# Performance work log

Hardware: AMD Instinct MI355X
Metric: run time of the kernel (lower is better)

The kernel has to match this reference:

```python
import jax, jax.numpy as jnp
import numpy as np

DIM = 256
HEADS = 8
KS = 3          # deform conv kernel size
N = KS * KS     # sampling points per output pixel
PAD = 1


def conv2d(x, w, b=None, stride=1, padding=0):
    out = jax.lax.conv_general_dilated(
        x, w, (stride, stride), [(padding, padding)] * 2,
        dimension_numbers=('NCHW', 'OIHW', 'NCHW'))
    if b is not None:
        out = out + b[None, :, None, None]
    return out


def deform_conv(x, w_pconv, b_pconv, w_dconv):
    b, c, h, w = x.shape
    offset = conv2d(x, w_pconv, b_pconv, padding=1)      # (b, 2N, h, w)
    off = offset.transpose(0, 2, 3, 1)                   # (b, h, w, 2N); [:N]=x-off, [N:]=y-off
    xp = jnp.pad(x, ((0, 0), (0, 0), (PAD, PAD), (PAD, PAD)))
    hp, wp = h + 2 * PAD, w + 2 * PAD
    r = jnp.arange(-(KS - 1) // 2, (KS - 1) // 2 + 1, dtype=x.dtype)
    pnx, pny = jnp.meshgrid(r, r, indexing='ij')
    # sampling positions, 1-indexed into the padded input (matches the torch ref)
    px = off[..., :N] + pnx.reshape(-1) + jnp.arange(1, h + 1, dtype=x.dtype)[None, :, None, None]
    py = off[..., N:] + pny.reshape(-1) + jnp.arange(1, w + 1, dtype=x.dtype)[None, None, :, None]
    fx = jnp.floor(px)
    fy = jnp.floor(py)
    qlt_x = jnp.clip(fx, 0, hp - 1)
    qlt_y = jnp.clip(fy, 0, wp - 1)
    qrb_x = jnp.clip(fx + 1, 0, hp - 1)
    qrb_y = jnp.clip(fy + 1, 0, wp - 1)
    pxc = jnp.clip(px, 0, hp - 1)
    pyc = jnp.clip(py, 0, wp - 1)
    # bilinear weights (can be negative at clamped borders, as in the torch ref)
    g_lt = (1 + (qlt_x - pxc)) * (1 + (qlt_y - pyc))
    g_rb = (1 - (qrb_x - pxc)) * (1 - (qrb_y - pyc))
    g_lb = (1 + (qlt_x - pxc)) * (1 - (qrb_y - pyc))
    g_rt = (1 - (qrb_x - pxc)) * (1 + (qlt_y - pyc))
    ilt_x = qlt_x.astype(jnp.int32)
    ilt_y = qlt_y.astype(jnp.int32)
    irb_x = qrb_x.astype(jnp.int32)
    irb_y = qrb_y.astype(jnp.int32)

    def gather(xb, ix, iy):
        return xb[:, ix, iy]                              # (c, h, w, N)

    gat = jax.vmap(gather)
    x_lt = gat(xp, ilt_x, ilt_y)
    x_rb = gat(xp, irb_x, irb_y)
    x_lb = gat(xp, ilt_x, irb_y)
    x_rt = gat(xp, irb_x, ilt_y)
    x_off = (g_lt[:, None] * x_lt + g_rb[:, None] * x_rb
             + g_lb[:, None] * x_lb + g_rt[:, None] * x_rt)   # (b, c, h, w, N)
    # 'b c h w (i j) -> b c (h i) (w j)' then ks-strided conv
    x_off = x_off.reshape(b, c, h, w, KS, KS).transpose(0, 1, 2, 4, 3, 5)
    x_off = x_off.reshape(b, c, h * KS, w * KS)
    return conv2d(x_off, w_dconv, None, stride=KS)


def ssa_forward(x, w_pconv, b_pconv, w_dconv, w_qkv, temperature, w_proj):
    b, c, h, w = x.shape
    hw = h * w
    ch = c // HEADS
    q = deform_conv(x, w_pconv, b_pconv, w_dconv)         # (b, c, h, w)
    qkv = jnp.einsum('bchw,oc->bohw', x, w_qkv)           # 1x1 conv, (b, 3c, h, w)
    k = qkv[:, c:2 * c]
    v = qkv[:, 2 * c:]
    q = q.reshape(b, HEADS, ch, hw)
    k = k.reshape(b, HEADS, ch, hw)
    v = v.reshape(b, HEADS, ch, hw)
    k = k / jnp.maximum(jnp.linalg.norm(k, axis=-1, keepdims=True), 1e-12)
    v = v / jnp.maximum(jnp.linalg.norm(v, axis=-1, keepdims=True), 1e-12)
    attn = jnp.einsum('bhcn,bhdn->bhcd', q, k) * temperature[None]   # (b, h, ch, ch)
    attn = jax.nn.softmax(attn, axis=-1)
    out = jnp.einsum('bhcd,bhdn->bhcn', attn, v).reshape(b, c, h, w)
    return jnp.einsum('bchw,oc->bohw', out, w_proj)       # project_out 1x1


def setup_inputs() -> dict:
    key = jax.random.key(0)
    ks = jax.random.split(key, 6)
    B, H, W = 2, 96, 96
    x = jax.random.normal(ks[0], (B, DIM, H, W), jnp.float32)
    w_pconv = jax.random.normal(ks[1], (2 * N, DIM, KS, KS), jnp.float32) * 0.01
    b_pconv = jax.random.normal(ks[2], (2 * N,), jnp.float32) * 0.01
    w_dconv = jax.random.normal(ks[3], (DIM, DIM, KS, KS), jnp.float32) * 0.02
    w_qkv = jax.random.normal(ks[4], (3 * DIM, DIM), jnp.float32) * 0.05
    temperature = jnp.ones((HEADS, 1, 1), jnp.float32)
    w_proj = jax.random.normal(ks[5], (DIM, DIM), jnp.float32) * 0.05
    return dict(x=x, w_pconv=w_pconv, b_pconv=b_pconv, w_dconv=w_dconv,
                w_qkv=w_qkv, temperature=temperature, w_proj=w_proj)


def reference(x, w_pconv, b_pconv, w_dconv, w_qkv, temperature, w_proj):
    return ssa_forward(x, w_pconv, b_pconv, w_dconv, w_qkv, temperature, w_proj)
```

## Files before the change

### kernel.cpp

```cpp
#include <hip/hip_runtime.h>
#include <math.h>

#define BB 2
#define CC 256
#define HW 96
#define PP 9216
#define KO 18
#define HEADS 8
#define NCH 18

typedef short bf16x8 __attribute__((ext_vector_type(8)));
typedef float f32x4 __attribute__((ext_vector_type(4)));

#define NP_O    0UL
#define W2_O    147456UL
#define IDX_O   331776UL
#define WGT_O   995328UL
#define WT2_O   1658880UL
#define WP2_O   2248704UL
#define WQ2_O   2322432UL
#define QP_O    2584576UL
#define KV_O    12021760UL
#define AP_O    21459968UL

__device__ __forceinline__ ushort f2bf_rne(float f) {
    unsigned u = __float_as_uint(f);
    unsigned r = (u + 0x7FFFu + ((u >> 16) & 1u)) >> 16;
    return (ushort)r;
}
__device__ __forceinline__ float bf2f(ushort h) {
    return __uint_as_float(((unsigned)h) << 16);
}

__global__ __launch_bounds__(256) void k_prep_wt(const float* __restrict__ wd,
                                                 ushort* __restrict__ h,
                                                 ushort* __restrict__ lo) {
    int tid = blockIdx.x * 256 + threadIdx.x;
    if (tid >= 9 * 8 * 1024 * 8) return;
    int e = tid & 7;
    int u = (tid >> 3) & 1023;
    int cs = (tid >> 13) & 7;
    int kk = tid >> 16;
    int oh = u >> 6, rem = u & 63;
    int lrow = rem & 15, lhi = rem >> 4;
    int o = oh * 16 + lrow;
    int c = cs * 32 + lhi * 8 + e;
    float v = wd[o * 2304 + c * 9 + kk];
    ushort hh = f2bf_rne(v);
    h[tid] = hh;
    lo[tid] = f2bf_rne(v - bf2f(hh));
}

__global__ __launch_bounds__(256) void k_prep_wp(const float* __restrict__ wp,
                                                 ushort* __restrict__ h,
                                                 ushort* __restrict__ lo) {
    int tid = blockIdx.x * 256 + threadIdx.x;
    if (tid >= 9 * 8 * 128 * 8) return;
    int e = tid & 7;
    int u = (tid >> 3) & 127;
    int cs = (tid >> 10) & 7;
    int kk = tid >> 13;
    int mf = u >> 6, rem = u & 63;
    int lrow = rem & 15, lhi = rem >> 4;
    int o = mf * 16 + lrow;
    int c = cs * 32 + lhi * 8 + e;
    float v = (o < KO) ? wp[(o * 256 + c) * 9 + kk] : 0.f;
    ushort hh = f2bf_rne(v);
    h[tid] = hh;
    lo[tid] = f2bf_rne(v - bf2f(hh));
}

__global__ __launch_bounds__(256) void k_prep_w(const float* __restrict__ W,
                                                ushort* __restrict__ h,
                                                ushort* __restrict__ lo,
                                                int total) {
    int tid = blockIdx.x * 256 + threadIdx.x;
    if (tid >= total) return;
    int e = tid & 7;
    int u = (tid >> 3) & 1023;
    int csg = (tid >> 13) & 7;
    int mt = tid >> 16;
    int rem = u & 63;
    int lrow = rem & 15, lhi = rem >> 4;
    int o = mt * 256 + (u >> 6) * 16 + lrow;
    int c = csg * 32 + lhi * 8 + e;
    float v = W[o * 256 + c];
    ushort hh = f2bf_rne(v);
    h[tid] = hh;
    lo[tid] = f2bf_rne(v - bf2f(hh));
}

__global__ __launch_bounds__(256) void k_xt(const float* __restrict__ x,
                                            float* __restrict__ xT) {
    int pt = blockIdx.x;
    int ct = blockIdx.y;
    int b  = blockIdx.z;
    int t = threadIdx.x;
    __shared__ float T[64][65];
    {
        int c = t >> 2, pq = (t & 3) * 16;
        const float* src = x + ((size_t)b * CC + ct * 64 + c) * PP + pt * 64 + pq;
#pragma unroll
        for (int k2 = 0; k2 < 4; ++k2) {
            float4 v = *(const float4*)&src[k2 * 4];
            T[c][pq + k2 * 4 + 0] = v.x;
            T[c][pq + k2 * 4 + 1] = v.y;
            T[c][pq + k2 * 4 + 2] = v.z;
            T[c][pq + k2 * 4 + 3] = v.w;
        }
    }
    __syncthreads();
    {
        int p = t >> 2, cq = (t & 3) * 16;
        float* dst = xT + ((size_t)b * PP + pt * 64 + p) * CC + ct * 64 + cq;
#pragma unroll
        for (int k2 = 0; k2 < 4; ++k2)
            *(float4*)&dst[k2 * 4] = make_float4(T[cq + k2 * 4 + 0][p], T[cq + k2 * 4 + 1][p],
                                                 T[cq + k2 * 4 + 2][p], T[cq + k2 * 4 + 3][p]);
    }
}

__global__ __launch_bounds__(256) void k_pconv(const float* __restrict__ x,
                                               const ushort* __restrict__ wp2h,
                                               const ushort* __restrict__ wp2l,
                                               float* __restrict__ ppart) {
    int s = blockIdx.x;
    int xcd = s & 7;
    int b = xcd & 1, ks = xcd >> 1;
    int p0 = (s >> 3) * 64;
    int t = threadIdx.x;
    int l = t & 63, w = t >> 6;
    int lrow = l & 15, lhi = l >> 4;
    int p = t & 63, cg = t >> 6;
    __shared__ __align__(16) ushort Sh[64 * 40];
    __shared__ __align__(16) ushort Sl[64 * 40];
    f32x4 acc[2];
    acc[0] = (f32x4)0.f; acc[1] = (f32x4)0.f;
    const float* xb = x + (size_t)b * CC * PP;
    int pix = p0 + p;
    int i_ = pix / 96, j_ = pix % 96;
#pragma unroll 1
    for (int cs = 0; cs < 2; ++cs) {
        int csg = ks * 2 + cs;
        const float* xc0 = xb + (size_t)(csg * 32 + cg * 8) * PP;
#pragma unroll 1
        for (int kk = 0; kk < 9; ++kk) {
            int di = kk / 3 - 1, dj = kk % 3 - 1;
            bool vOK = ((unsigned)(i_ + di) < 96u) && ((unsigned)(j_ + dj) < 96u);
            int poff = pix + di * 96 + dj;
            __syncthreads();
            bf16x8 ah[2], al[2];
#pragma unroll
            for (int mf = 0; mf < 2; ++mf) {
                size_t gi = (((size_t)(kk * 8 + csg)) * 128 + (mf * 64 + l)) * 8;
                ah[mf] = *(const bf16x8*)&wp2h[gi];
                al[mf] = *(const bf16x8*)&wp2l[gi];
            }
            bf16x8 vh, vl;
#pragma unroll
            for (int i = 0; i < 8; ++i) {
                float v = vOK ? xc0[(size_t)i * PP + poff] : 0.f;
                ushort hh = f2bf_rne(v);
                vh[i] = (short)hh;
                vl[i] = (short)f2bf_rne(v - bf2f(hh));
            }
            *(bf16x8*)&Sh[p * 40 + cg * 8] = vh;
            *(bf16x8*)&Sl[p * 40 + cg * 8] = vl;
            __syncthreads();
            bf16x8 Bh = *(const bf16x8*)&Sh[(w * 16 + lrow) * 40 + lhi * 8];
            bf16x8 Bl = *(const bf16x8*)&Sl[(w * 16 + lrow) * 40 + lhi * 8];
#pragma unroll
            for (int mf = 0; mf < 2; ++mf) {
                acc[mf] = __builtin_amdgcn_mfma_f32_16x16x32_bf16(ah[mf], Bh, acc[mf], 0, 0, 0);
                acc[mf] = __builtin_amdgcn_mfma_f32_16x16x32_bf16(ah[mf], Bl, acc[mf], 0, 0, 0);
                acc[mf] = __builtin_amdgcn_mfma_f32_16x16x32_bf16(al[mf], Bh, acc[mf], 0, 0, 0);
            }
        }
    }
    float* pr = ppart + ((size_t)(ks * BB + b) * 32) * PP;
#pragma unroll
    for (int mf = 0; mf < 2; ++mf)
#pragma unroll
        for (int j = 0; j < 4; ++j)
            pr[(size_t)(mf * 16 + lhi * 4 + j) * PP + p0 + w * 16 + lrow] = acc[mf][j];
}

__global__ __launch_bounds__(256) void k_bilin2(const float* __restrict__ pp,
                                                const float* __restrict__ bp,
                                                int4* __restrict__ idx4,
                                                float4* __restrict__ wgt4) {
    int idx = blockIdx.x * 256 + threadIdx.x;
    if (idx >= BB * 9 * PP) return;
    int p = idx % PP;
    int bn = idx / PP;
    int n = bn % 9, b = bn / 9;
    int i = p / 96, j = p % 96;
    float ox = bp[n], oy = bp[n + 9];
#pragma unroll
    for (int k = 0; k < 4; ++k) {
        ox += pp[((size_t)(k * BB + b) * 32 + n) * PP + p];
        oy += pp[((size_t)(k * BB + b) * 32 + n + 9) * PP + p];
    }
    float px = ox + (float)(n / 3 - 1) + (float)(i + 1);
    float py = oy + (float)(n % 3 - 1) + (float)(j + 1);
    float fx = floorf(px), fy = floorf(py);
    float qltx = fminf(fmaxf(fx, 0.f), 97.f);
    float qlty = fminf(fmaxf(fy, 0.f), 97.f);
    float qrbx = fminf(fmaxf(fx + 1.f, 0.f), 97.f);
    float qrby = fminf(fmaxf(fy + 1.f, 0.f), 97.f);
    float pxc = fminf(fmaxf(px, 0.f), 97.f);
    float pyc = fminf(fmaxf(py, 0.f), 97.f);
    float glt = (1.f + (qltx - pxc)) * (1.f + (qlty - pyc));
    float grb = (1.f - (qrbx - pxc)) * (1.f - (qrby - pyc));
    float glb = (1.f + (qltx - pxc)) * (1.f - (qrby - pyc));
    float grt = (1.f - (qrbx - pxc)) * (1.f + (qlty - pyc));
    int x0 = (int)qltx - 1, y0 = (int)qlty - 1;
    int x1 = (int)qrbx - 1, y1 = (int)qrby - 1;
    bool vlt = (x0 >= 0 && x0 < 96 && y0 >= 0 && y0 < 96);
    bool vrb = (x1 >= 0 && x1 < 96 && y1 >= 0 && y1 < 96);
    bool vlb = (x0 >= 0 && x0 < 96 && y1 >= 0 && y1 < 96);
    bool vrt = (x1 >= 0 && x1 < 96 && y0 >= 0 && y0 < 96);
    int4 id;
    id.x = vlt ? x0 * 96 + y0 : 0;
    id.y = vrb ? x1 * 96 + y1 : 0;
    id.z = vlb ? x0 * 96 + y1 : 0;
    id.w = vrt ? x1 * 96 + y0 : 0;
    idx4[idx] = id;
    wgt4[idx] = make_float4(vlt ? glt : 0.f, vrb ? grb : 0.f,
                            vlb ? glb : 0.f, vrt ? grt : 0.f);
}

__global__ __launch_bounds__(256) void k_dconv(const float* __restrict__ xT,
                                               const ushort* __restrict__ wt2h,
                                               const ushort* __restrict__ wt2l,
                                               const int4* __restrict__ idx4,
                                               const float4* __restrict__ wgt4,
                                               float* __restrict__ qpart) {
    int s = blockIdx.x;
    int xcd = s & 7, ib = s >> 3;
    int combo = xcd >> 1;
    int b = combo & 1;
    int half = combo >> 1;
    int ptile = (xcd & 1) * 144 + ib;
    int p0 = ptile * 32;
    int t = threadIdx.x;
    int l = t & 63, w = t >> 6;
    int lrow = l & 15, lhi = l >> 4;
    int obase = w * 64;
    int pl = t & 31, cg = t >> 5;

    __shared__ __align__(16) ushort Sh0[32 * 40], Sl0[32 * 40];
    __shared__ __align__(16) ushort Sh1[32 * 40], Sl1[32 * 40];
    __shared__ int4 Tid[9 * 32];
    __shared__ float4 Twg[9 * 32];

    for (int e = t; e < 9 * 32; e += 256) {
        int kk = e >> 5, pq = e & 31;
        size_t tb = ((size_t)b * 9 + kk) * PP + p0 + pq;
        Tid[e] = idx4[tb];
        Twg[e] = wgt4[tb];
    }

    f32x4 acc[4][2];
#pragma unroll
    for (int mf = 0; mf < 4; ++mf)
#pragma unroll
        for (int nf = 0; nf < 2; ++nf) acc[mf][nf] = (f32x4)0.f;

    const float* xTb = xT + (size_t)b * PP * CC;
    int h4 = half * 4;

    float R[16];
    float4 g4r;

    auto LD = [&](int i) {
        int cs = i / 9, kk = i % 9;
        int csg = h4 + cs;
        int4 id = Tid[kk * 32 + pl];
        g4r = Twg[kk * 32 + pl];
        const float* xt0 = xTb + (size_t)(csg * 32 + cg * 4);
        *(float4*)&R[0]  = *(const float4*)&xt0[(size_t)id.x * CC];
        *(float4*)&R[4]  = *(const float4*)&xt0[(size_t)id.y * CC];
        *(float4*)&R[8]  = *(const float4*)&xt0[(size_t)id.z * CC];
        *(float4*)&R[12] = *(const float4*)&xt0[(size_t)id.w * CC];
    };
    auto CONV = [&](ushort* Sh, ushort* Sl) {
        ushort4 vh, vl;
#pragma unroll
        for (int q = 0; q < 4; ++q) {
            float v = g4r.x * R[q];
            v = fmaf(g4r.y, R[4 + q], v);
            v = fmaf(g4r.z, R[8 + q], v);
            v = fmaf(g4r.w, R[12 + q], v);
            ushort hh = f2bf_rne(v);
            ushort ll = f2bf_rne(v - bf2f(hh));
            if (q == 0)      { vh.x = hh; vl.x = ll; }
            else if (q == 1) { vh.y = hh; vl.y = ll; }
            else if (q == 2) { vh.z = hh; vl.z = ll; }
            else             { vh.w = hh; vl.w = ll; }
        }
        *(ushort4*)&Sh[pl * 40 + cg * 4] = vh;
        *(ushort4*)&Sl[pl * 40 + cg * 4] = vl;
    };
    auto COMPUTE = [&](int i, const ushort* Sh, const ushort* Sl) {
        int cs = i / 9, kk = i % 9;
        int csg = h4 + cs;
        bf16x8 ah[4], al[4];
#pragma unroll
        for (int mf = 0; mf < 4; ++mf) {
            size_t gi = (((size_t)(kk * 8 + csg)) * 1024 + ((w * 4 + mf) * 64 + l)) * 8;
            ah[mf] = *(const bf16x8*)&wt2h[gi];
            al[mf] = *(const bf16x8*)&wt2l[gi];
        }
        bf16x8 Bh2[2], Bl2[2];
#pragma unroll
        for (int nf = 0; nf < 2; ++nf) {
            Bh2[nf] = *(const bf16x8*)&Sh[(nf * 16 + lrow) * 40 + lhi * 8];
            Bl2[nf] = *(const bf16x8*)&Sl[(nf * 16 + lrow) * 40 + lhi * 8];
        }
        __builtin_amdgcn_s_setprio(1);
#pragma unroll
        for (int mf = 0; mf < 4; ++mf)
#pragma unroll
            for (int nf = 0; nf < 2; ++nf) {
                acc[mf][nf] = __builtin_amdgcn_mfma_f32_16x16x32_bf16(ah[mf], Bh2[nf], acc[mf][nf], 0, 0, 0);
                acc[mf][nf] = __builtin_amdgcn_mfma_f32_16x16x32_bf16(ah[mf], Bl2[nf], acc[mf][nf], 0, 0, 0);
                acc[mf][nf] = __builtin_amdgcn_mfma_f32_16x16x32_bf16(al[mf], Bh2[nf], acc[mf][nf], 0, 0, 0);
            }
        __builtin_amdgcn_s_setprio(0);
    };

    __syncthreads();
    LD(0); CONV(Sh0, Sl0);
    LD(1);
    __syncthreads();

#pragma unroll 1
    for (int i0 = 0; i0 < 36; i0 += 2) {
        CONV(Sh1, Sl1);
        if (i0 + 2 < 36) LD(i0 + 2);
        COMPUTE(i0, Sh0, Sl0);
        __syncthreads();
        if (i0 + 2 < 36) CONV(Sh0, Sl0);
        if (i0 + 3 < 36) LD(i0 + 3);
        COMPUTE(i0 + 1, Sh1, Sl1);
        __syncthreads();
    }

    float* qh = qpart + (size_t)half * BB * CC * PP + (size_t)b * CC * PP;
#pragma unroll
    for (int mf = 0; mf < 4; ++mf)
#pragma unroll
        for (int nf = 0; nf < 2; ++nf)
#pragma unroll
            for (int j = 0; j < 4; ++j)
                qh[(size_t)(obase + mf * 16 + lhi * 4 + j) * PP + p0 + nf * 16 + lrow] =
                    acc[mf][nf][j];
}

__global__ __launch_bounds__(256) void k_gemm_bf(const float* __restrict__ Bsrc,
                                                 const ushort* __restrict__ A2h,
                                                 const ushort* __restrict__ A2l,
                                                 float* __restrict__ C,
                                                 int mtiles, int bRowStride, int bRowOff,
                                                 int aBatchStride,
                                                 float* __restrict__ npart) {
    int s = blockIdx.x;
    int xcd = s & 7, ib = s >> 3;
    int b, mt, ptile;
    if (mtiles == 2) {
        int combo = xcd >> 1;
        b = combo & 1; mt = combo >> 1;
        ptile = (xcd & 1) * 72 + ib;
    } else {
        b = xcd >> 2; mt = 0;
        ptile = (xcd & 3) * 36 + ib;
    }
    int p0 = ptile * 64;
    int t = threadIdx.x;
    int l = t & 63, w = t >> 6;
    int lrow = l & 15, lhi = l >> 4;
    int obase = w * 64;
    int p = t & 63, cg = t >> 6;
    __shared__ __align__(16) ushort Sh[64 * 40];
    __shared__ __align__(16) ushort Sl[64 * 40];
    f32x4 acc[4][4];
#pragma unroll
    for (int mf = 0; mf < 4; ++mf)
#pragma unroll
        for (int nf = 0; nf < 4; ++nf) acc[mf][nf] = (f32x4)0.f;
    const float* Bb = Bsrc + ((size_t)b * bRowStride + bRowOff) * PP;
    const ushort* Ah = A2h + (size_t)b * aBatchStride;
    const ushort* Al = A2l + (size_t)b * aBatchStride;
#pragma unroll 1
    for (int csg = 0; csg < 8; ++csg) {
        __syncthreads();
        bf16x8 ah[4], al[4];
#pragma unroll
        for (int mf = 0; mf < 4; ++mf) {
            size_t gi = (((size_t)(mt * 8 + csg)) * 1024 + ((w * 4 + mf) * 64 + l)) * 8;
            ah[mf] = *(const bf16x8*)&Ah[gi];
            al[mf] = *(const bf16x8*)&Al[gi];
        }
        const float* xr = Bb + (size_t)(csg * 32 + cg * 8) * PP + p0 + p;
        bf16x8 vh, vl;
#pragma unroll
        for (int i = 0; i < 8; ++i) {
            float v = xr[(size_t)i * PP];
            ushort hh = f2bf_rne(v);
            vh[i] = (short)hh;
            vl[i] = (short)f2bf_rne(v - bf2f(hh));
        }
        *(bf16x8*)&Sh[p * 40 + cg * 8] = vh;
        *(bf16x8*)&Sl[p * 40 + cg * 8] = vl;
        __syncthreads();
        bf16x8 Bh4[4], Bl4[4];
#pragma unroll
        for (int nf = 0; nf < 4; ++nf) {
            Bh4[nf] = *(const bf16x8*)&Sh[(nf * 16 + lrow) * 40 + lhi * 8];
            Bl4[nf] = *(const bf16x8*)&Sl[(nf * 16 + lrow) * 40 + lhi * 8];
        }
#pragma unroll
        for (int mf = 0; mf < 4; ++mf) {
#pragma unroll
            for (int nf = 0; nf < 4; ++nf) {
                acc[mf][nf] = __builtin_amdgcn_mfma_f32_16x16x32_bf16(ah[mf], Bh4[nf], acc[mf][nf], 0, 0, 0);
                acc[mf][nf] = __builtin_amdgcn_mfma_f32_16x16x32_bf16(ah[mf], Bl4[nf], acc[mf][nf], 0, 0, 0);
                acc[mf][nf] = __builtin_amdgcn_mfma_f32_16x16x32_bf16(al[mf], Bh4[nf], acc[mf][nf], 0, 0, 0);
            }
        }
    }
    float* Cb = C + (size_t)b * (mtiles * 256) * PP;
#pragma unroll
    for (int mf = 0; mf < 4; ++mf)
#pragma unroll
        for (int nf = 0; nf < 4; ++nf)
#pragma unroll
            for (int j = 0; j < 4; ++j)
                Cb[(size_t)(mt * 256 + obase + mf * 16 + lhi * 4 + j) * PP + p0 + nf * 16 + lrow] =
                    acc[mf][nf][j];
    if (npart) {
        float sq[4][4];
#pragma unroll
        for (int mf = 0; mf < 4; ++mf)
#pragma unroll
            for (int j = 0; j < 4; ++j) {
                float v0 = acc[mf][0][j], v1 = acc[mf][1][j];
                float v2 = acc[mf][2][j], v3 = acc[mf][3][j];
                sq[mf][j] = v0 * v0 + v1 * v1 + v2 * v2 + v3 * v3;
            }
#pragma unroll
        for (int m = 1; m <= 8; m <<= 1)
#pragma unroll
            for (int mf = 0; mf < 4; ++mf)
#pragma unroll
                for (int j = 0; j < 4; ++j)
                    sq[mf][j] += __shfl_xor(sq[mf][j], m, 64);
        if (lrow == 0) {
            float* np = npart + ((size_t)(b * 2 + mt) * 144 + ptile) * 256;
#pragma unroll
            for (int mf = 0; mf < 4; ++mf)
#pragma unroll
                for (int j = 0; j < 4; ++j)
                    np[obase + mf * 16 + lhi * 4 + j] = sq[mf][j];
        }
    }
}

__global__ __launch_bounds__(256) void k_attn_part(const float* __restrict__ qp,
                                                   const float* __restrict__ kv,
                                                   float* __restrict__ apart) {
    int ch = blockIdx.x, h = blockIdx.y, b = blockIdx.z;
    int t = threadIdx.x;
    int d = t & 31, cg = t >> 5;
    __shared__ float qs[32][37], ks[32][37];
    float acc[4] = {0.f, 0.f, 0.f, 0.f};
    const float* q0 = qp + ((size_t)b * CC + h * 32) * PP;
    const float* q1 = q0 + (size_t)BB * CC * PP;
    const float* kb = kv + ((size_t)b * 512 + h * 32) * PP;
    int r = t >> 3, cq = (t & 7) * 4;
    for (int po = ch * 512; po < ch * 512 + 512; po += 32) {
        float4 va = *(const float4*)&q0[(size_t)r * PP + po + cq];
        float4 vb = *(const float4*)&q1[(size_t)r * PP + po + cq];
        qs[r][cq + 0] = va.x + vb.x; qs[r][cq + 1] = va.y + vb.y;
        qs[r][cq + 2] = va.z + vb.z; qs[r][cq + 3] = va.w + vb.w;
        float4 vk = *(const float4*)&kb[(size_t)r * PP + po + cq];
        ks[r][cq + 0] = vk.x; ks[r][cq + 1] = vk.y;
        ks[r][cq + 2] = vk.z; ks[r][cq + 3] = vk.w;
        __syncthreads();
#pragma unroll
        for (int pq = 0; pq < 32; ++pq) {
            float kvv = ks[d][pq];
#pragma unroll
            for (int i = 0; i < 4; ++i)
                acc[i] = fmaf(qs[cg * 4 + i][pq], kvv, acc[i]);
        }
        __syncthreads();
    }
    float* ap = apart + (((size_t)(b * 8 + h) * NCH + ch) << 10);
#pragma unroll
    for (int i = 0; i < 4; ++i) ap[(cg * 4 + i) * 32 + d] = acc[i];
}

__global__ __launch_bounds__(256) void k_attn_fin_w2(const float* __restrict__ apart,
                                                     const float* __restrict__ npart,
                                                     const float* __restrict__ temp,
                                                     const float* __restrict__ wproj,
                                                     ushort* __restrict__ w2h,
                                                     ushort* __restrict__ w2l) {
    int h = blockIdx.x, b = blockIdx.y;
    int t = threadIdx.x;
    __shared__ float A[32][33];
    __shared__ float invk[32], invv[32];
    if (t < 64) {
        int mt = t >> 5, row = (t & 31) + h * 32;
        const float* base = npart + ((size_t)(b * 2 + mt) * 144) * 256 + row;
        float ssum = 0.f;
        for (int pt = 0; pt < 144; ++pt) ssum += base[pt * 256];
        float iv = 1.f / fmaxf(sqrtf(ssum), 1e-12f);
        if (mt == 0) invk[t & 31] = iv; else invv[t & 31] = iv;
    }
    const float* ap = apart + ((size_t)(b * 8 + h) * NCH << 10);
    float th = temp[h];
    for (int e = t; e < 1024; e += 256) {
        float s = 0.f;
        for (int chn = 0; chn < NCH; ++chn) s += ap[chn * 1024 + e];
        A[e >> 5][e & 31] = s * th;
    }
    __syncthreads();
    if (t < 32) {
        int c = t;
        float m = -INFINITY;
        float row[32];
#pragma unroll
        for (int d = 0; d < 32; ++d) {
            row[d] = A[c][d] * invk[d];
            m = fmaxf(m, row[d]);
        }
        float sum = 0.f;
#pragma unroll
        for (int d = 0; d < 32; ++d) sum += expf(row[d] - m);
        float inv = 1.f / sum;
#pragma unroll
        for (int d = 0; d < 32; ++d)
            A[c][d] = expf(row[d] - m) * inv * invv[d];
    }
    __syncthreads();
    int o = t;
    float wrow[32];
#pragma unroll
    for (int c = 0; c < 32; ++c) wrow[c] = wproj[o * 256 + h * 32 + c];
    int wq = o >> 6, mf = (o >> 4) & 3, lr = o & 15;
    size_t bb = (size_t)b * 65536;
#pragma unroll
    for (int e = 0; e < 32; ++e) {
        float v = 0.f;
#pragma unroll
        for (int c = 0; c < 32; ++c) v = fmaf(wrow[c], A[c][e], v);
        int lhi = e >> 3, ee = e & 7;
        size_t gi = bb + ((size_t)h * 1024 + ((wq * 4 + mf) * 64 + lhi * 16 + lr)) * 8 + ee;
        ushort hh = f2bf_rne(v);
        w2h[gi] = hh;
        w2l[gi] = f2bf_rne(v - bf2f(hh));
    }
}

extern "C" void kernel_launch(void* const* d_in, const int* in_sizes, int n_in,
                              void* d_out, int out_size, void* d_ws, size_t ws_size,
                              hipStream_t stream) {
    const float* x     = (const float*)d_in[0];
    const float* wp    = (const float*)d_in[1];
    const float* bp    = (const float*)d_in[2];
    const float* wd    = (const float*)d_in[3];
    const float* wqkv  = (const float*)d_in[4];
    const float* temp  = (const float*)d_in[5];
    const float* wproj = (const float*)d_in[6];
    float* out = (float*)d_out;
    float* ws  = (float*)d_ws;

    float* npart  = ws + NP_O;
    ushort* w2h   = (ushort*)(ws + W2_O);
    ushort* w2l   = w2h + 2 * 65536;
    int4*  idx4   = (int4*)(ws + IDX_O);
    float4* wgt4  = (float4*)(ws + WGT_O);
    ushort* wt2h  = (ushort*)(ws + WT2_O);
    ushort* wt2l  = wt2h + 9 * 8 * 1024 * 8;
    ushort* wp2h  = (ushort*)(ws + WP2_O);
    ushort* wp2l  = wp2h + 9 * 8 * 128 * 8;
    ushort* wq2h  = (ushort*)(ws + WQ2_O);
    ushort* wq2l  = wq2h + 2 * 8 * 1024 * 8;
    float* qpart  = ws + QP_O;
    float* ppart  = ws + QP_O;
    float* xT     = ws + KV_O;
    float* kv     = ws + KV_O;
    float* apart  = ws + AP_O;

    k_prep_wt<<<2304, 256, 0, stream>>>(wd, wt2h, wt2l);
    k_prep_wp<<<288, 256, 0, stream>>>(wp, wp2h, wp2l);
    k_prep_w<<<512, 256, 0, stream>>>(wqkv + 256 * 256, wq2h, wq2l, 2 * 65536);
    k_pconv<<<1152, 256, 0, stream>>>(x, wp2h, wp2l, ppart);
    k_bilin2<<<(BB * 9 * PP + 255) / 256, 256, 0, stream>>>(ppart, bp, idx4, wgt4);
    k_xt<<<dim3(144, 4, BB), 256, 0, stream>>>(x, xT);
    k_dconv<<<1152, 256, 0, stream>>>(xT, wt2h, wt2l, idx4, wgt4, qpart);
    k_gemm_bf<<<576, 256, 0, stream>>>(x, wq2h, wq2l, kv, 2, 256, 0, 0, npart);
    k_attn_part<<<dim3(NCH, HEADS, BB), 256, 0, stream>>>(qpart, kv, apart);
    k_attn_fin_w2<<<dim3(HEADS, BB), 256, 0, stream>>>(apart, npart, temp, wproj, w2h, w2l);
    k_gemm_bf<<<288, 256, 0, stream>>>(kv, w2h, w2l, out, 1, 512, 256, 65536, nullptr);
}
```

Baseline: 267.3 us.

## Merge prep and bilinear/transpose launches; deepen dconv gather pipeline to two stages

The three weight-prep kernels become one launch that dispatches by block index, and the bilinear-index kernel and the x transpose kernel are merged into another. This removes launch gaps and lets independent work share one grid. In the deformable conv, the LDS ring grows to four buffers and two gather loads are issued per phase, so gathers for steps i+4 and i+5 are in flight while two MFMA steps run, with one barrier per two steps. The cost is more registers and LDS per block, which may lower occupancy.

```diff
diff --git a/kernel.cpp b/kernel.cpp
--- a/kernel.cpp
+++ b/kernel.cpp
@@ -32,91 +32,56 @@
     return __uint_as_float(((unsigned)h) << 16);
 }
 
-__global__ __launch_bounds__(256) void k_prep_wt(const float* __restrict__ wd,
-                                                 ushort* __restrict__ h,
-                                                 ushort* __restrict__ lo) {
-    int tid = blockIdx.x * 256 + threadIdx.x;
-    if (tid >= 9 * 8 * 1024 * 8) return;
-    int e = tid & 7;
-    int u = (tid >> 3) & 1023;
-    int cs = (tid >> 13) & 7;
-    int kk = tid >> 16;
-    int oh = u >> 6, rem = u & 63;
-    int lrow = rem & 15, lhi = rem >> 4;
-    int o = oh * 16 + lrow;
-    int c = cs * 32 + lhi * 8 + e;
-    float v = wd[o * 2304 + c * 9 + kk];
-    ushort hh = f2bf_rne(v);
-    h[tid] = hh;
-    lo[tid] = f2bf_rne(v - bf2f(hh));
-}
-
-__global__ __launch_bounds__(256) void k_prep_wp(const float* __restrict__ wp,
-                                                 ushort* __restrict__ h,
-                                                 ushort* __restrict__ lo) {
-    int tid = blockIdx.x * 256 + threadIdx.x;
-    if (tid >= 9 * 8 * 128 * 8) return;
-    int e = tid & 7;
-    int u = (tid >> 3) & 127;
-    int cs = (tid >> 10) & 7;
-    int kk = tid >> 13;
-    int mf = u >> 6, rem = u & 63;
-    int lrow = rem & 15, lhi = rem >> 4;
-    int o = mf * 16 + lrow;
-    int c = cs * 32 + lhi * 8 + e;
-    float v = (o < KO) ? wp[(o * 256 + c) * 9 + kk] : 0.f;
-    ushort hh = f2bf_rne(v);
-    h[tid] = hh;
-    lo[tid] = f2bf_rne(v - bf2f(hh));
-}
-
-__global__ __launch_bounds__(256) void k_prep_w(const float* __restrict__ W,
-                                                ushort* __restrict__ h,
-                                                ushort* __restrict__ lo,
-                                                int total) {
-    int tid = blockIdx.x * 256 + threadIdx.x;
-    if (tid >= total) return;
-    int e = tid & 7;
-    int u = (tid >> 3) & 1023;
-    int csg = (tid >> 13) & 7;
-    int mt = tid >> 16;
-    int rem = u & 63;
-    int lrow = rem & 15, lhi = rem >> 4;
-    int o = mt * 256 + (u >> 6) * 16 + lrow;
-    int c = csg * 32 + lhi * 8 + e;
-    float v = W[o * 256 + c];
-    ushort hh = f2bf_rne(v);
-    h[tid] = hh;
-    lo[tid] = f2bf_rne(v - bf2f(hh));
-}
-
-__global__ __launch_bounds__(256) void k_xt(const float* __restrict__ x,
-                                            float* __restrict__ xT) {
-    int pt = blockIdx.x;
-    int ct = blockIdx.y;
-    int b  = blockIdx.z;
+__global__ __launch_bounds__(256) void k_prep_all(const float* __restrict__ wd,
+                                                  const float* __restrict__ wp,
+                                                  const float* __restrict__ wqk,
+                                                  ushort* __restrict__ wt2h, ushort* __restrict__ wt2l,
+                                                  ushort* __restrict__ wp2h, ushort* __restrict__ wp2l,
+                                                  ushort* __restrict__ wq2h, ushort* __restrict__ wq2l) {
+    int blk = blockIdx.x;
     int t = threadIdx.x;
-    __shared__ float T[64][65];
-    {
-        int c = t >> 2, pq = (t & 3) * 16;
-        const float* src = x + ((size_t)b * CC + ct * 64 + c) * PP + pt * 64 + pq;
-#pragma unroll
-        for (int k2 = 0; k2 < 4; ++k2) {
-            float4 v = *(const float4*)&src[k2 * 4];
-            T[c][pq + k2 * 4 + 0] = v.x;
-            T[c][pq + k2 * 4 + 1] = v.y;
-            T[c][pq + k2 * 4 + 2] = v.z;
-            T[c][pq + k2 * 4 + 3] = v.w;
-        }
-    }
-    __syncthreads();
-    {
-        int p = t >> 2, cq = (t & 3) * 16;
-        float* dst = xT + ((size_t)b * PP + pt * 64 + p) * CC + ct * 64 + cq;
-#pragma unroll
-        for (int k2 = 0; k2 < 4; ++k2)
-            *(float4*)&dst[k2 * 4] = make_float4(T[cq + k2 * 4 + 0][p], T[cq + k2 * 4 + 1][p],
-                                                 T[cq + k2 * 4 + 2][p], T[cq + k2 * 4 + 3][p]);
+    if (blk < 2304) {
+        int tid = blk * 256 + t;
+        int e = tid & 7;
+        int u = (tid >> 3) & 1023;
+        int cs = (tid >> 13) & 7;
+        int kk = tid >> 16;
+        int oh = u >> 6, rem = u & 63;
+        int lrow = rem & 15, lhi = rem >> 4;
+        int o = oh * 16 + lrow;
+        int c = cs * 32 + lhi * 8 + e;
+        float v = wd[o * 2304 + c * 9 + kk];
+        ushort hh = f2bf_rne(v);
+        wt2h[tid] = hh;
+        wt2l[tid] = f2bf_rne(v - bf2f(hh));
+    } else if (blk < 2592) {
+        int tid = (blk - 2304) * 256 + t;
+        int e = tid & 7;
+        int u = (tid >> 3) & 127;
+        int cs = (tid >> 10) & 7;
+        int kk = tid >> 13;
+        int mf = u >> 6, rem = u & 63;
+        int lrow = rem & 15, lhi = rem >> 4;
+        int o = mf * 16 + lrow;
+        int c = cs * 32 + lhi * 8 + e;
+        float v = (o < KO) ? wp[(o * 256 + c) * 9 + kk] : 0.f;
+        ushort hh = f2bf_rne(v);
+        wp2h[tid] = hh;
+        wp2l[tid] = f2bf_rne(v - bf2f(hh));
+    } else {
+        int tid = (blk - 2592) * 256 + t;
+        int e = tid & 7;
+        int u = (tid >> 3) & 1023;
+        int csg = (tid >> 13) & 7;
+        int mt = tid >> 16;
+        int rem = u & 63;
+        int lrow = rem & 15, lhi = rem >> 4;
+        int o = mt * 256 + (u >> 6) * 16 + lrow;
+        int c = csg * 32 + lhi * 8 + e;
+        float v = wqk[o * 256 + c];
+        ushort hh = f2bf_rne(v);
+        wq2h[tid] = hh;
+        wq2l[tid] = f2bf_rne(v - bf2f(hh));
     }
 }
 
@@ -185,49 +150,82 @@
             pr[(size_t)(mf * 16 + lhi * 4 + j) * PP + p0 + w * 16 + lrow] = acc[mf][j];
 }
 
-__global__ __launch_bounds__(256) void k_bilin2(const float* __restrict__ pp,
-                                                const float* __restrict__ bp,
-                                                int4* __restrict__ idx4,
-                                                float4* __restrict__ wgt4) {
-    int idx = blockIdx.x * 256 + threadIdx.x;
-    if (idx >= BB * 9 * PP) return;
-    int p = idx % PP;
-    int bn = idx / PP;
-    int n = bn % 9, b = bn / 9;
-    int i = p / 96, j = p % 96;
-    float ox = bp[n], oy = bp[n + 9];
-#pragma unroll
-    for (int k = 0; k < 4; ++k) {
-        ox += pp[((size_t)(k * BB + b) * 32 + n) * PP + p];
-        oy += pp[((size_t)(k * BB + b) * 32 + n + 9) * PP + p];
-    }
-    float px = ox + (float)(n / 3 - 1) + (float)(i + 1);
-    float py = oy + (float)(n % 3 - 1) + (float)(j + 1);
-    float fx = floorf(px), fy = floorf(py);
-    float qltx = fminf(fmaxf(fx, 0.f), 97.f);
-    float qlty = fminf(fmaxf(fy, 0.f), 97.f);
-    float qrbx = fminf(fmaxf(fx + 1.f, 0.f), 97.f);
-    float qrby = fminf(fmaxf(fy + 1.f, 0.f), 97.f);
-    float pxc = fminf(fmaxf(px, 0.f), 97.f);
-    float pyc = fminf(fmaxf(py, 0.f), 97.f);
-    float glt = (1.f + (qltx - pxc)) * (1.f + (qlty - pyc));
-    float grb = (1.f - (qrbx - pxc)) * (1.f - (qrby - pyc));
-    float glb = (1.f + (qltx - pxc)) * (1.f - (qrby - pyc));
-    float grt = (1.f - (qrbx - pxc)) * (1.f + (qlty - pyc));
-    int x0 = (int)qltx - 1, y0 = (int)qlty - 1;
-    int x1 = (int)qrbx - 1, y1 = (int)qrby - 1;
-    bool vlt = (x0 >= 0 && x0 < 96 && y0 >= 0 && y0 < 96);
-    bool vrb = (x1 >= 0 && x1 < 96 && y1 >= 0 && y1 < 96);
-    bool vlb = (x0 >= 0 && x0 < 96 && y1 >= 0 && y1 < 96);
-    bool vrt = (x1 >= 0 && x1 < 96 && y0 >= 0 && y0 < 96);
-    int4 id;
-    id.x = vlt ? x0 * 96 + y0 : 0;
-    id.y = vrb ? x1 * 96 + y1 : 0;
-    id.z = vlb ? x0 * 96 + y1 : 0;
-    id.w = vrt ? x1 * 96 + y0 : 0;
-    idx4[idx] = id;
-    wgt4[idx] = make_float4(vlt ? glt : 0.f, vrb ? grb : 0.f,
-                            vlb ? glb : 0.f, vrt ? grt : 0.f);
+__global__ __launch_bounds__(256) void k_bilin_xt(const float* __restrict__ pp,
+                                                  const float* __restrict__ bp,
+                                                  int4* __restrict__ idx4,
+                                                  float4* __restrict__ wgt4,
+                                                  const float* __restrict__ x,
+                                                  float* __restrict__ xT) {
+    int blk = blockIdx.x;
+    int t = threadIdx.x;
+    if (blk < 648) {
+        int idx = blk * 256 + t;
+        if (idx >= BB * 9 * PP) return;
+        int p = idx % PP;
+        int bn = idx / PP;
+        int n = bn % 9, b = bn / 9;
+        int i = p / 96, j = p % 96;
+        float ox = bp[n], oy = bp[n + 9];
+#pragma unroll
+        for (int k = 0; k < 4; ++k) {
+            ox += pp[((size_t)(k * BB + b) * 32 + n) * PP + p];
+            oy += pp[((size_t)(k * BB + b) * 32 + n + 9) * PP + p];
+        }
+        float px = ox + (float)(n / 3 - 1) + (float)(i + 1);
+        float py = oy + (float)(n % 3 - 1) + (float)(j + 1);
+        float fx = floorf(px), fy = floorf(py);
+        float qltx = fminf(fmaxf(fx, 0.f), 97.f);
+        float qlty = fminf(fmaxf(fy, 0.f), 97.f);
+        float qrbx = fminf(fmaxf(fx + 1.f, 0.f), 97.f);
+        float qrby = fminf(fmaxf(fy + 1.f, 0.f), 97.f);
+        float pxc = fminf(fmaxf(px, 0.f), 97.f);
+        float pyc = fminf(fmaxf(py, 0.f), 97.f);
+        float glt = (1.f + (qltx - pxc)) * (1.f + (qlty - pyc));
+        float grb = (1.f - (qrbx - pxc)) * (1.f - (qrby - pyc));
+        float glb = (1.f + (qltx - pxc)) * (1.f - (qrby - pyc));
+        float grt = (1.f - (qrbx - pxc)) * (1.f + (qlty - pyc));
+        int x0 = (int)qltx - 1, y0 = (int)qlty - 1;
+        int x1 = (int)qrbx - 1, y1 = (int)qrby - 1;
+        bool vlt = (x0 >= 0 && x0 < 96 && y0 >= 0 && y0 < 96);
+        bool vrb = (x1 >= 0 && x1 < 96 && y1 >= 0 && y1 < 96);
+        bool vlb = (x0 >= 0 && x0 < 96 && y1 >= 0 && y1 < 96);
+        bool vrt = (x1 >= 0 && x1 < 96 && y0 >= 0 && y0 < 96);
+        int4 id;
+        id.x = vlt ? x0 * 96 + y0 : 0;
+        id.y = vrb ? x1 * 96 + y1 : 0;
+        id.z = vlb ? x0 * 96 + y1 : 0;
+        id.w = vrt ? x1 * 96 + y0 : 0;
+        idx4[idx] = id;
+        wgt4[idx] = make_float4(vlt ? glt : 0.f, vrb ? grb : 0.f,
+                                vlb ? glb : 0.f, vrt ? grt : 0.f);
+    } else {
+        int s2 = blk - 648;
+        int pt = s2 % 144;
+        int ct = (s2 / 144) & 3;
+        int b = s2 / 576;
+        __shared__ float T[64][65];
+        {
+            int c = t >> 2, pq = (t & 3) * 16;
+            const float* src = x + ((size_t)b * CC + ct * 64 + c) * PP + pt * 64 + pq;
+#pragma unroll
+            for (int k2 = 0; k2 < 4; ++k2) {
+                float4 v = *(const float4*)&src[k2 * 4];
+                T[c][pq + k2 * 4 + 0] = v.x;
+                T[c][pq + k2 * 4 + 1] = v.y;
+                T[c][pq + k2 * 4 + 2] = v.z;
+                T[c][pq + k2 * 4 + 3] = v.w;
+            }
+        }
+        __syncthreads();
+        {
+            int p = t >> 2, cq = (t & 3) * 16;
+            float* dst = xT + ((size_t)b * PP + pt * 64 + p) * CC + ct * 64 + cq;
+#pragma unroll
+            for (int k2 = 0; k2 < 4; ++k2)
+                *(float4*)&dst[k2 * 4] = make_float4(T[cq + k2 * 4 + 0][p], T[cq + k2 * 4 + 1][p],
+                                                     T[cq + k2 * 4 + 2][p], T[cq + k2 * 4 + 3][p]);
+        }
+    }
 }
 
 __global__ __launch_bounds__(256) void k_dconv(const float* __restrict__ xT,
@@ -249,8 +247,7 @@
     int obase = w * 64;
     int pl = t & 31, cg = t >> 5;
 
-    __shared__ __align__(16) ushort Sh0[32 * 40], Sl0[32 * 40];
-    __shared__ __align__(16) ushort Sh1[32 * 40], Sl1[32 * 40];
+    __shared__ __align__(16) ushort SH[4][1280], SL[4][1280];
     __shared__ int4 Tid[9 * 32];
     __shared__ float4 Twg[9 * 32];
 
@@ -270,28 +267,28 @@
     const float* xTb = xT + (size_t)b * PP * CC;
     int h4 = half * 4;
 
-    float R[16];
-    float4 g4r;
-
-    auto LD = [&](int i) {
+    float R0[16], R1[16];
+    float4 g0, g1;
+
+    auto LD = [&](int i, float (&R)[16], float4& g) {
         int cs = i / 9, kk = i % 9;
         int csg = h4 + cs;
         int4 id = Tid[kk * 32 + pl];
-        g4r = Twg[kk * 32 + pl];
+        g = Twg[kk * 32 + pl];
         const float* xt0 = xTb + (size_t)(csg * 32 + cg * 4);
         *(float4*)&R[0]  = *(const float4*)&xt0[(size_t)id.x * CC];
         *(float4*)&R[4]  = *(const float4*)&xt0[(size_t)id.y * CC];
         *(float4*)&R[8]  = *(const float4*)&xt0[(size_t)id.z * CC];
         *(float4*)&R[12] = *(const float4*)&xt0[(size_t)id.w * CC];
     };
-    auto CONV = [&](ushort* Sh, ushort* Sl) {
+    auto CONV = [&](const float (&R)[16], float4 g, ushort* Sh, ushort* Sl) {
         ushort4 vh, vl;
 #pragma unroll
         for (int q = 0; q < 4; ++q) {
-            float v = g4r.x * R[q];
-            v = fmaf(g4r.y, R[4 + q], v);
-            v = fmaf(g4r.z, R[8 + q], v);
-            v = fmaf(g4r.w, R[12 + q], v);
+            float v = g.x * R[q];
+            v = fmaf(g.y, R[4 + q], v);
+            v = fmaf(g.z, R[8 + q], v);
+            v = fmaf(g.w, R[12 + q], v);
             ushort hh = f2bf_rne(v);
             ushort ll = f2bf_rne(v - bf2f(hh));
             if (q == 0)      { vh.x = hh; vl.x = ll; }
@@ -331,19 +328,23 @@
     };
 
     __syncthreads();
-    LD(0); CONV(Sh0, Sl0);
-    LD(1);
+    LD(0, R0, g0); LD(1, R1, g1);
+    CONV(R0, g0, SH[0], SL[0]);
+    CONV(R1, g1, SH[1], SL[1]);
+    LD(2, R0, g0); LD(3, R1, g1);
     __syncthreads();
 
 #pragma unroll 1
-    for (int i0 = 0; i0 < 36; i0 += 2) {
-        CONV(Sh1, Sl1);
-        if (i0 + 2 < 36) LD(i0 + 2);
-        COMPUTE(i0, Sh0, Sl0);
-        __syncthreads();
-        if (i0 + 2 < 36) CONV(Sh0, Sl0);
-        if (i0 + 3 < 36) LD(i0 + 3);
-        COMPUTE(i0 + 1, Sh1, Sl1);
+    for (int ph = 0; ph < 18; ++ph) {
+        int s0 = ph * 2;
+        int cur = (ph & 1) * 2;
+        int nxt = ((ph + 1) & 1) * 2;
+        if (s0 + 2 < 36) CONV(R0, g0, SH[nxt], SL[nxt]);
+        if (s0 + 3 < 36) CONV(R1, g1, SH[nxt + 1], SL[nxt + 1]);
+        if (s0 + 4 < 36) LD(s0 + 4, R0, g0);
+        if (s0 + 5 < 36) LD(s0 + 5, R1, g1);
+        COMPUTE(s0, SH[cur], SL[cur]);
+        COMPUTE(s0 + 1, SH[cur + 1], SL[cur + 1]);
         __syncthreads();
     }
 
@@ -595,12 +596,10 @@
     float* kv     = ws + KV_O;
     float* apart  = ws + AP_O;
 
-    k_prep_wt<<<2304, 256, 0, stream>>>(wd, wt2h, wt2l);
-    k_prep_wp<<<288, 256, 0, stream>>>(wp, wp2h, wp2l);
-    k_prep_w<<<512, 256, 0, stream>>>(wqkv + 256 * 256, wq2h, wq2l, 2 * 65536);
+    k_prep_all<<<3104, 256, 0, stream>>>(wd, wp, wqkv + 256 * 256,
+                                         wt2h, wt2l, wp2h, wp2l, wq2h, wq2l);
     k_pconv<<<1152, 256, 0, stream>>>(x, wp2h, wp2l, ppart);
-    k_bilin2<<<(BB * 9 * PP + 255) / 256, 256, 0, stream>>>(ppart, bp, idx4, wgt4);
-    k_xt<<<dim3(144, 4, BB), 256, 0, stream>>>(x, xT);
+    k_bilin_xt<<<1800, 256, 0, stream>>>(ppart, bp, idx4, wgt4, x, xT);
     k_dconv<<<1152, 256, 0, stream>>>(xT, wt2h, wt2l, idx4, wgt4, qpart);
     k_gemm_bf<<<576, 256, 0, stream>>>(x, wq2h, wq2l, kv, 2, 256, 0, 0, npart);
     k_attn_part<<<dim3(NCH, HEADS, BB), 256, 0, stream>>>(qpart, kv, apart);
```

Result: faster. 257.3 us (-3.7%).
